# Optimization experiments

Measured on AMD Instinct MI355X. Metric: run time of the kernel, lower is better.

## Reference

```python
import jax, jax.numpy as jnp
import numpy as np

BNH, L, D = 32, 1024, 64        # (b*nh, seq_len, d_k)
CLIP = 64                        # rel_pos_clip
R = 2 * CLIP + 1                 # rel-pos table rows = 129
TEMP = 8.0                       # temperature = sqrt(d_k)


def setup_inputs() -> dict:
    key = jax.random.key(0)
    ks = jax.random.split(key, 7)
    q = jax.random.normal(ks[0], (BNH, L, D), jnp.float32)
    k = jax.random.normal(ks[1], (BNH, L, D), jnp.float32)
    v = jax.random.normal(ks[2], (BNH, L, D), jnp.float32)
    attn_w = jax.random.normal(ks[3], (BNH, L, L), jnp.float32)
    emb_k = jax.random.normal(ks[4], (R, D), jnp.float32)
    emb_v = jax.random.normal(ks[5], (R, D), jnp.float32)
    pos_seqs = jnp.sort(jax.random.randint(ks[6], (BNH, L), 0, 2048), axis=-1)
    mask = jnp.zeros((BNH, L, L), dtype=bool)  # no positions masked
    return {"q": q, "k": k, "v": v, "attn_w": attn_w,
            "emb_k": emb_k, "emb_v": emb_v,
            "pos_seqs": pos_seqs, "mask": mask}


def reference(q, k, v, attn_w, emb_k, emb_v, pos_seqs, mask):
    # relative-position index table: table[b,j,k] = clip(pos[k]-pos[j]) + CLIP, in [0, 2*CLIP]
    table = jnp.clip(pos_seqs[:, None, :] - pos_seqs[:, :, None], -CLIP, CLIP) + CLIP  # (bnh,l,l)

    # content scores
    attn = jnp.einsum('bid,bjd->bij', q, k)  # (bnh,l,l)

    # rel-pos key term: einsum('ijm,ijkm->ijk', q, emb_k[table]) done WITHOUT
    # materializing the (bnh,l,l,d) gather: project q onto all R embeddings,
    # then gather along the R axis (same math, far less memory traffic).
    qe = jnp.einsum('bid,rd->bir', q, emb_k)                 # (bnh,l,R)
    attn = attn + jnp.take_along_axis(qe, table, axis=2)     # (bnh,l,l)

    # score_util == 'np': additive posterior scores
    attn = attn + attn_w

    attn = attn / TEMP
    attn = jnp.where(mask, -jnp.inf, attn)
    p = jax.nn.softmax(attn, axis=2)
    # dropout is identity in eval mode

    out = jnp.einsum('bij,bjd->bid', p, v)                   # (bnh,l,d)

    # rel-pos value term: einsum('ijk,ijkm->ijm', p, emb_v[table]) via
    # scatter-add of probs into R buckets, then one small GEMM.
    bi = jnp.arange(BNH)[:, None, None]
    li = jnp.arange(L)[None, :, None]
    av = jnp.zeros((BNH, L, R), p.dtype).at[bi, li, table].add(p)  # (bnh,l,R)
    out = out + jnp.einsum('bir,rd->bid', av, emb_v)
    return out, p
```

## Files before the change

kernel.cpp:

```cpp
#include <hip/hip_runtime.h>

#define BNH 32
#define L 1024
#define D 64
#define RP 129
#define CLIPV 64
#define TI 16
#define TJ 128
#define NJT (L / TJ)
#define NT 256
#define SS 1032
#define KST 72
#define VST 136

typedef __attribute__((ext_vector_type(8))) short bf16x8;
typedef __attribute__((ext_vector_type(4))) float f32x4;
typedef __attribute__((ext_vector_type(8))) _Float16 f16x8;
typedef __attribute__((ext_vector_type(4))) _Float16 f16x4;

__device__ __forceinline__ unsigned short f2bf(float f) {
    unsigned int u = __builtin_bit_cast(unsigned int, f);
    return (unsigned short)((u + 0x7fffu + ((u >> 16) & 1u)) >> 16);
}

__global__ __launch_bounds__(NT, 2) void attn_fused(
    const float* __restrict__ q, const float* __restrict__ k, const float* __restrict__ v,
    const float* __restrict__ attn_w, const float* __restrict__ emb_k,
    const float* __restrict__ emb_v, const int* __restrict__ pos,
    const unsigned char* __restrict__ mask,
    float* __restrict__ out, float* __restrict__ p_out) {

    __shared__ __attribute__((aligned(16))) _Float16 s_lds[TI][SS];
    __shared__ __attribute__((aligned(16))) unsigned short kv_u[TJ * KST];
    __shared__ __attribute__((aligned(16))) unsigned short q_u[TI * KST];
    __shared__ unsigned short pos_s[L];
    __shared__ float qeav_s[TI * RP];
    __shared__ __attribute__((aligned(16))) float qfout_s[TI * 68];
    __shared__ float m_part[4][16];
    __shared__ float m_s[16];
    __shared__ float l_s[16];

    const int tid = threadIdx.x;
    const int wg = ((int)blockIdx.x & 7) * ((BNH * (L / TI)) >> 3) + ((int)blockIdx.x >> 3);
    const int b = wg >> 6;
    const int i0 = (wg & 63) * TI;
    const int w = tid >> 6;
    const int lane = tid & 63;
    const int quad = lane >> 4;
    const int lo = lane & 15;

    for (int t = tid; t < L; t += NT) pos_s[t] = (unsigned short)pos[b * L + t];
    {
        const int row = tid >> 4, c4 = tid & 15;
        *reinterpret_cast<float4*>(&qfout_s[row * 68 + c4 * 4]) =
            *reinterpret_cast<const float4*>(q + ((size_t)(b * L + i0 + row)) * D + c4 * 4);
    }
    if (tid < TI * 8) {
        const int r = tid >> 3, dc = tid & 7;
        const float* src = q + ((size_t)(b * L + i0 + r)) * D + dc * 8;
        float4 f0 = *(const float4*)src;
        float4 f1 = *(const float4*)(src + 4);
        bf16x8 qq;
        qq[0] = (short)f2bf(f0.x); qq[1] = (short)f2bf(f0.y);
        qq[2] = (short)f2bf(f0.z); qq[3] = (short)f2bf(f0.w);
        qq[4] = (short)f2bf(f1.x); qq[5] = (short)f2bf(f1.y);
        qq[6] = (short)f2bf(f1.z); qq[7] = (short)f2bf(f1.w);
        *(bf16x8*)&q_u[r * KST + dc * 8] = qq;
    }
    __syncthreads();

    {
        const int row = tid >> 4, rr = tid & 15;
        for (int r = rr; r < RP; r += 16) {
            float acc = 0.f;
#pragma unroll
            for (int d4 = 0; d4 < 16; ++d4) {
                float4 qv = *reinterpret_cast<const float4*>(&qfout_s[row * 68 + d4 * 4]);
                float4 ev = *reinterpret_cast<const float4*>(emb_k + r * D + d4 * 4);
                acc += qv.x * ev.x + qv.y * ev.y + qv.z * ev.z + qv.w * ev.w;
            }
            qeav_s[row * RP + r] = acc;
        }
    }
    __syncthreads();

    const bf16x8 aq0 = *(const bf16x8*)&q_u[lo * KST + quad * 8];
    const bf16x8 aq1 = *(const bf16x8*)&q_u[lo * KST + 32 + quad * 8];

    int posA[4];
#pragma unroll
    for (int r = 0; r < 4; ++r) posA[r] = (int)pos_s[i0 + quad * 4 + r];

    float mA[4] = {-3e38f, -3e38f, -3e38f, -3e38f};
    for (int jt = 0; jt < NJT; ++jt) {
        const int j0 = jt * TJ;
#pragma unroll
        for (int s = 0; s < 4; ++s) {
            int ch = s * NT + tid;
            int col = ch >> 3, dc = ch & 7;
            const float* src = k + ((size_t)(b * L + j0 + col)) * D + dc * 8;
            float4 f0 = *(const float4*)src;
            float4 f1 = *(const float4*)(src + 4);
            bf16x8 kk;
            kk[0] = (short)f2bf(f0.x); kk[1] = (short)f2bf(f0.y);
            kk[2] = (short)f2bf(f0.z); kk[3] = (short)f2bf(f0.w);
            kk[4] = (short)f2bf(f1.x); kk[5] = (short)f2bf(f1.y);
            kk[6] = (short)f2bf(f1.z); kk[7] = (short)f2bf(f1.w);
            *(bf16x8*)&kv_u[col * KST + dc * 8] = kk;
        }
        __syncthreads();
#pragma unroll
        for (int ct = 0; ct < 2; ++ct) {
            const int ncol = w * 32 + ct * 16 + lo;
            const int j = j0 + ncol;
            bf16x8 b0 = *(const bf16x8*)&kv_u[ncol * KST + quad * 8];
            bf16x8 b1 = *(const bf16x8*)&kv_u[ncol * KST + 32 + quad * 8];
            f32x4 acc = {0.f, 0.f, 0.f, 0.f};
            acc = __builtin_amdgcn_mfma_f32_16x16x32_bf16(aq0, b0, acc, 0, 0, 0);
            acc = __builtin_amdgcn_mfma_f32_16x16x32_bf16(aq1, b1, acc, 0, 0, 0);
            const int pj = (int)pos_s[j];
#pragma unroll
            for (int r = 0; r < 4; ++r) {
                const int row = quad * 4 + r;
                const size_t grow = (size_t)(b * L + i0 + row) * L + j;
                int dd = pj - posA[r];
                dd = min(max(dd, -CLIPV), CLIPV) + CLIPV;
                float sc = (acc[r] + qeav_s[row * RP + dd] + attn_w[grow]) * 0.125f;
                if (mask[grow]) sc = -3e38f;
                mA[r] = fmaxf(mA[r], sc);
                s_lds[row][j] = (_Float16)sc;
            }
        }
        __syncthreads();
    }

#pragma unroll
    for (int off = 1; off < 16; off <<= 1) {
#pragma unroll
        for (int r = 0; r < 4; ++r) mA[r] = fmaxf(mA[r], __shfl_xor(mA[r], off, 64));
    }
    if (lo == 0) {
#pragma unroll
        for (int r = 0; r < 4; ++r) m_part[w][quad * 4 + r] = mA[r];
    }
    __syncthreads();
    if (tid < 16) {
        m_s[tid] = fmaxf(fmaxf(m_part[0][tid], m_part[1][tid]),
                         fmaxf(m_part[2][tid], m_part[3][tid]));
        l_s[tid] = 0.f;
    }
    for (int t = tid; t < TI * RP; t += NT) qeav_s[t] = 0.f;
    for (int t = tid; t < TI * 68; t += NT) qfout_s[t] = 0.f;
    __syncthreads();

    const float mrow = m_s[lo];
    const int pos_m = (int)pos_s[i0 + lo];
    float l_r = 0.f;
    f32x4 oc[4];
#pragma unroll
    for (int ct = 0; ct < 4; ++ct) { oc[ct][0]=0.f; oc[ct][1]=0.f; oc[ct][2]=0.f; oc[ct][3]=0.f; }

    for (int jt = 0; jt < NJT; ++jt) {
        const int j0 = jt * TJ;
        const int colv = tid & 127, hv = tid >> 7;
        const float* srcv = v + ((size_t)(b * L + j0 + colv)) * D + hv * 32;
        float4 vf[8];
#pragma unroll
        for (int s = 0; s < 8; ++s) vf[s] = *(const float4*)(srcv + s * 4);
        __syncthreads();
#pragma unroll
        for (int s = 0; s < 8; ++s) {
            const int dbase = hv * 32 + s * 4;
            kv_u[(dbase + 0) * VST + colv] = f2bf(vf[s].x);
            kv_u[(dbase + 1) * VST + colv] = f2bf(vf[s].y);
            kv_u[(dbase + 2) * VST + colv] = f2bf(vf[s].z);
            kv_u[(dbase + 3) * VST + colv] = f2bf(vf[s].w);
        }
        __syncthreads();

        const int jcol = j0 + w * 32 + quad * 8;
        f16x8 sv = *reinterpret_cast<const f16x8*>(&s_lds[lo][jcol]);
        float ev[8];
#pragma unroll
        for (int i = 0; i < 8; ++i) ev[i] = __expf((float)sv[i] - mrow);
        l_r += ev[0] + ev[1] + ev[2] + ev[3] + ev[4] + ev[5] + ev[6] + ev[7];
        int cur = -1; float a = 0.f;
#pragma unroll
        for (int i = 0; i < 8; ++i) {
            int dd = (int)pos_s[jcol + i] - pos_m;
            dd = min(max(dd, -CLIPV), CLIPV) + CLIPV;
            if (dd != cur) {
                if (cur >= 0) atomicAdd(&qeav_s[lo * RP + cur], a);
                cur = dd; a = 0.f;
            }
            a += ev[i];
        }
        atomicAdd(&qeav_s[lo * RP + cur], a);
        bf16x8 af;
#pragma unroll
        for (int i = 0; i < 8; ++i) af[i] = (short)f2bf(ev[i]);
#pragma unroll
        for (int ct = 0; ct < 4; ++ct) {
            bf16x8 bf = *reinterpret_cast<const bf16x8*>(
                &kv_u[(ct * 16 + lo) * VST + w * 32 + quad * 8]);
            oc[ct] = __builtin_amdgcn_mfma_f32_16x16x32_bf16(af, bf, oc[ct], 0, 0, 0);
        }
    }

#pragma unroll
    for (int ct = 0; ct < 4; ++ct) {
#pragma unroll
        for (int r = 0; r < 4; ++r)
            atomicAdd(&qfout_s[(quad * 4 + r) * 68 + ct * 16 + lo], oc[ct][r]);
    }
    l_r += __shfl_xor(l_r, 16, 64);
    l_r += __shfl_xor(l_r, 32, 64);
    if (lane < 16) atomicAdd(&l_s[lo], l_r);
    __syncthreads();
    if (tid < 16) l_s[tid] = 1.f / l_s[tid];
    __syncthreads();

#pragma unroll
    for (int s = 0; s < TI; ++s) {
        f16x4 sv = *reinterpret_cast<const f16x4*>(&s_lds[s][tid * 4]);
        const float mm = m_s[s], il = l_s[s];
        float4 pv;
        pv.x = __expf((float)sv[0] - mm) * il;
        pv.y = __expf((float)sv[1] - mm) * il;
        pv.z = __expf((float)sv[2] - mm) * il;
        pv.w = __expf((float)sv[3] - mm) * il;
        *reinterpret_cast<float4*>(p_out + (size_t)(b * L + i0 + s) * L + tid * 4) = pv;
    }

    {
        const int row = tid >> 4, dc = tid & 15;
        float4 o = *(const float4*)&qfout_s[row * 68 + dc * 4];
        const float il = l_s[row];
        for (int r = 0; r < RP; ++r) {
            float a = qeav_s[row * RP + r];
            if (a != 0.f) {
                const float4 ev4 = *(const float4*)(emb_v + r * D + dc * 4);
                o.x += a * ev4.x; o.y += a * ev4.y;
                o.z += a * ev4.z; o.w += a * ev4.w;
            }
        }
        o.x *= il; o.y *= il; o.z *= il; o.w *= il;
        *(float4*)(out + (size_t)(b * L + i0 + row) * D + dc * 4) = o;
    }
}

extern "C" void kernel_launch(void* const* d_in, const int* in_sizes, int n_in,
                              void* d_out, int out_size, void* d_ws, size_t ws_size,
                              hipStream_t stream) {
    const float* q = (const float*)d_in[0];
    const float* k = (const float*)d_in[1];
    const float* v = (const float*)d_in[2];
    const float* attn_w = (const float*)d_in[3];
    const float* emb_k = (const float*)d_in[4];
    const float* emb_v = (const float*)d_in[5];
    const int* pos = (const int*)d_in[6];
    const unsigned char* mask = (const unsigned char*)d_in[7];
    float* out = (float*)d_out;
    float* p_out = out + (size_t)BNH * L * D;

    attn_fused<<<BNH * (L / TI), NT, 0, stream>>>(q, k, v, attn_w, emb_k, emb_v,
                                                  pos, mask, out, p_out);
}
```

Measured before the change: 647.6 us.

## Give each wave a private K/V tile with register double-buffering and cut shared memory

```diff
diff --git a/kernel.cpp b/kernel.cpp
--- a/kernel.cpp
+++ b/kernel.cpp
@@ -6,12 +6,12 @@
 #define RP 129
 #define CLIPV 64
 #define TI 16
-#define TJ 128
+#define TJ 64
 #define NJT (L / TJ)
 #define NT 256
 #define SS 1032
-#define KST 72
-#define VST 136
+#define KVST 72
+#define VTST 40
 
 typedef __attribute__((ext_vector_type(8))) short bf16x8;
 typedef __attribute__((ext_vector_type(4))) float f32x4;
@@ -23,22 +23,25 @@
     return (unsigned short)((u + 0x7fffu + ((u >> 16) & 1u)) >> 16);
 }
 
-__global__ __launch_bounds__(NT, 2) void attn_fused(
+__global__ __launch_bounds__(NT, 3) void attn_fused(
     const float* __restrict__ q, const float* __restrict__ k, const float* __restrict__ v,
     const float* __restrict__ attn_w, const float* __restrict__ emb_k,
     const float* __restrict__ emb_v, const int* __restrict__ pos,
     const unsigned char* __restrict__ mask,
     float* __restrict__ out, float* __restrict__ p_out) {
 
-    __shared__ __attribute__((aligned(16))) _Float16 s_lds[TI][SS];
-    __shared__ __attribute__((aligned(16))) unsigned short kv_u[TJ * KST];
-    __shared__ __attribute__((aligned(16))) unsigned short q_u[TI * KST];
-    __shared__ unsigned short pos_s[L];
-    __shared__ float qeav_s[TI * RP];
-    __shared__ __attribute__((aligned(16))) float qfout_s[TI * 68];
-    __shared__ float m_part[4][16];
-    __shared__ float m_s[16];
-    __shared__ float l_s[16];
+    __shared__ __attribute__((aligned(16))) char smem[53952];
+    _Float16* s_h = (_Float16*)smem;
+    float* qf = (float*)smem;
+    float* embv = (float*)smem;
+    unsigned short* kv = (unsigned short*)(smem + 33024);
+    float* buf0 = (float*)(smem + 33024);
+    float* buf1 = (float*)(smem + 37376);
+    float* qeav = (float*)(smem + 43264);
+    unsigned short* pos_s = (unsigned short*)(smem + 51520);
+    float* m_part = (float*)(smem + 53568);
+    float* m_s = (float*)(smem + 53824);
+    float* l_s = (float*)(smem + 53888);
 
     const int tid = threadIdx.x;
     const int wg = ((int)blockIdx.x & 7) * ((BNH * (L / TI)) >> 3) + ((int)blockIdx.x >> 3);
@@ -48,24 +51,13 @@
     const int lane = tid & 63;
     const int quad = lane >> 4;
     const int lo = lane & 15;
+    unsigned short* kvw = kv + w * 1280;
 
     for (int t = tid; t < L; t += NT) pos_s[t] = (unsigned short)pos[b * L + t];
     {
         const int row = tid >> 4, c4 = tid & 15;
-        *reinterpret_cast<float4*>(&qfout_s[row * 68 + c4 * 4]) =
+        *reinterpret_cast<float4*>(&qf[row * 68 + c4 * 4]) =
             *reinterpret_cast<const float4*>(q + ((size_t)(b * L + i0 + row)) * D + c4 * 4);
-    }
-    if (tid < TI * 8) {
-        const int r = tid >> 3, dc = tid & 7;
-        const float* src = q + ((size_t)(b * L + i0 + r)) * D + dc * 8;
-        float4 f0 = *(const float4*)src;
-        float4 f1 = *(const float4*)(src + 4);
-        bf16x8 qq;
-        qq[0] = (short)f2bf(f0.x); qq[1] = (short)f2bf(f0.y);
-        qq[2] = (short)f2bf(f0.z); qq[3] = (short)f2bf(f0.w);
-        qq[4] = (short)f2bf(f1.x); qq[5] = (short)f2bf(f1.y);
-        qq[6] = (short)f2bf(f1.z); qq[7] = (short)f2bf(f1.w);
-        *(bf16x8*)&q_u[r * KST + dc * 8] = qq;
     }
     __syncthreads();
 
@@ -75,63 +67,96 @@
             float acc = 0.f;
 #pragma unroll
             for (int d4 = 0; d4 < 16; ++d4) {
-                float4 qv = *reinterpret_cast<const float4*>(&qfout_s[row * 68 + d4 * 4]);
+                float4 qv = *reinterpret_cast<const float4*>(&qf[row * 68 + d4 * 4]);
                 float4 ev = *reinterpret_cast<const float4*>(emb_k + r * D + d4 * 4);
                 acc += qv.x * ev.x + qv.y * ev.y + qv.z * ev.z + qv.w * ev.w;
             }
-            qeav_s[row * RP + r] = acc;
-        }
-    }
-    __syncthreads();
-
-    const bf16x8 aq0 = *(const bf16x8*)&q_u[lo * KST + quad * 8];
-    const bf16x8 aq1 = *(const bf16x8*)&q_u[lo * KST + 32 + quad * 8];
-
+            qeav[row * RP + r] = acc;
+        }
+    }
+
+    bf16x8 aq0, aq1;
+    {
+        const float* qrow = q + (size_t)(b * L + i0 + lo) * D + quad * 8;
+        float4 a0 = *(const float4*)qrow, a1 = *(const float4*)(qrow + 4);
+        float4 a2 = *(const float4*)(qrow + 32), a3 = *(const float4*)(qrow + 36);
+        aq0[0] = (short)f2bf(a0.x); aq0[1] = (short)f2bf(a0.y);
+        aq0[2] = (short)f2bf(a0.z); aq0[3] = (short)f2bf(a0.w);
+        aq0[4] = (short)f2bf(a1.x); aq0[5] = (short)f2bf(a1.y);
+        aq0[6] = (short)f2bf(a1.z); aq0[7] = (short)f2bf(a1.w);
+        aq1[0] = (short)f2bf(a2.x); aq1[1] = (short)f2bf(a2.y);
+        aq1[2] = (short)f2bf(a2.z); aq1[3] = (short)f2bf(a2.w);
+        aq1[4] = (short)f2bf(a3.x); aq1[5] = (short)f2bf(a3.y);
+        aq1[6] = (short)f2bf(a3.z); aq1[7] = (short)f2bf(a3.w);
+    }
     int posA[4];
 #pragma unroll
     for (int r = 0; r < 4; ++r) posA[r] = (int)pos_s[i0 + quad * 4 + r];
+    __syncthreads();
 
     float mA[4] = {-3e38f, -3e38f, -3e38f, -3e38f};
-    for (int jt = 0; jt < NJT; ++jt) {
+
+    auto LOADA = [&](float4* kr, float* awr, int* mkr, int jt) {
         const int j0 = jt * TJ;
-#pragma unroll
-        for (int s = 0; s < 4; ++s) {
-            int ch = s * NT + tid;
-            int col = ch >> 3, dc = ch & 7;
-            const float* src = k + ((size_t)(b * L + j0 + col)) * D + dc * 8;
-            float4 f0 = *(const float4*)src;
-            float4 f1 = *(const float4*)(src + 4);
+        const int jj = j0 + w * 16 + lo;
+#pragma unroll
+        for (int r = 0; r < 4; ++r) {
+            const size_t grow = (size_t)(b * L + i0 + quad * 4 + r) * L + jj;
+            awr[r] = attn_w[grow];
+            mkr[r] = (int)mask[grow];
+        }
+#pragma unroll
+        for (int c = 0; c < 2; ++c) {
+            const int ch = c * 64 + lane;
+            const int col = ch >> 3, dc = ch & 7;
+            const float* src = k + ((size_t)(b * L + j0 + w * 16 + col)) * D + dc * 8;
+            kr[c * 2 + 0] = *(const float4*)src;
+            kr[c * 2 + 1] = *(const float4*)(src + 4);
+        }
+    };
+    auto PROCA = [&](const float4* kr, const float* awr, const int* mkr, int jt) {
+        const int j0 = jt * TJ;
+#pragma unroll
+        for (int c = 0; c < 2; ++c) {
+            const int ch = c * 64 + lane;
+            const int col = ch >> 3, dc = ch & 7;
             bf16x8 kk;
-            kk[0] = (short)f2bf(f0.x); kk[1] = (short)f2bf(f0.y);
-            kk[2] = (short)f2bf(f0.z); kk[3] = (short)f2bf(f0.w);
-            kk[4] = (short)f2bf(f1.x); kk[5] = (short)f2bf(f1.y);
-            kk[6] = (short)f2bf(f1.z); kk[7] = (short)f2bf(f1.w);
-            *(bf16x8*)&kv_u[col * KST + dc * 8] = kk;
-        }
-        __syncthreads();
-#pragma unroll
-        for (int ct = 0; ct < 2; ++ct) {
-            const int ncol = w * 32 + ct * 16 + lo;
-            const int j = j0 + ncol;
-            bf16x8 b0 = *(const bf16x8*)&kv_u[ncol * KST + quad * 8];
-            bf16x8 b1 = *(const bf16x8*)&kv_u[ncol * KST + 32 + quad * 8];
-            f32x4 acc = {0.f, 0.f, 0.f, 0.f};
-            acc = __builtin_amdgcn_mfma_f32_16x16x32_bf16(aq0, b0, acc, 0, 0, 0);
-            acc = __builtin_amdgcn_mfma_f32_16x16x32_bf16(aq1, b1, acc, 0, 0, 0);
-            const int pj = (int)pos_s[j];
-#pragma unroll
-            for (int r = 0; r < 4; ++r) {
-                const int row = quad * 4 + r;
-                const size_t grow = (size_t)(b * L + i0 + row) * L + j;
-                int dd = pj - posA[r];
-                dd = min(max(dd, -CLIPV), CLIPV) + CLIPV;
-                float sc = (acc[r] + qeav_s[row * RP + dd] + attn_w[grow]) * 0.125f;
-                if (mask[grow]) sc = -3e38f;
-                mA[r] = fmaxf(mA[r], sc);
-                s_lds[row][j] = (_Float16)sc;
-            }
-        }
-        __syncthreads();
+            kk[0] = (short)f2bf(kr[c * 2].x);     kk[1] = (short)f2bf(kr[c * 2].y);
+            kk[2] = (short)f2bf(kr[c * 2].z);     kk[3] = (short)f2bf(kr[c * 2].w);
+            kk[4] = (short)f2bf(kr[c * 2 + 1].x); kk[5] = (short)f2bf(kr[c * 2 + 1].y);
+            kk[6] = (short)f2bf(kr[c * 2 + 1].z); kk[7] = (short)f2bf(kr[c * 2 + 1].w);
+            *(bf16x8*)&kvw[col * KVST + dc * 8] = kk;
+        }
+        bf16x8 b0 = *(const bf16x8*)&kvw[lo * KVST + quad * 8];
+        bf16x8 b1 = *(const bf16x8*)&kvw[lo * KVST + 32 + quad * 8];
+        f32x4 acc = {0.f, 0.f, 0.f, 0.f};
+        acc = __builtin_amdgcn_mfma_f32_16x16x32_bf16(aq0, b0, acc, 0, 0, 0);
+        acc = __builtin_amdgcn_mfma_f32_16x16x32_bf16(aq1, b1, acc, 0, 0, 0);
+        const int j = j0 + w * 16 + lo;
+        const int pj = (int)pos_s[j];
+#pragma unroll
+        for (int r = 0; r < 4; ++r) {
+            const int row = quad * 4 + r;
+            int dd = pj - posA[r];
+            dd = min(max(dd, -CLIPV), CLIPV) + CLIPV;
+            float sc = (acc[r] + qeav[row * RP + dd] + awr[r]) * 0.125f;
+            if (mkr[r]) sc = -3e38f;
+            mA[r] = fmaxf(mA[r], sc);
+            s_h[row * SS + j] = (_Float16)sc;
+        }
+    };
+
+    {
+        float4 krA[4], krB[4];
+        float awA[4], awB[4];
+        int mkA[4], mkB[4];
+        LOADA(krA, awA, mkA, 0);
+        for (int jt = 0; jt < NJT; jt += 2) {
+            LOADA(krB, awB, mkB, jt + 1);
+            PROCA(krA, awA, mkA, jt);
+            if (jt + 2 < NJT) LOADA(krA, awA, mkA, jt + 2);
+            PROCA(krB, awB, mkB, jt + 1);
+        }
     }
 
 #pragma unroll
@@ -141,88 +166,95 @@
     }
     if (lo == 0) {
 #pragma unroll
-        for (int r = 0; r < 4; ++r) m_part[w][quad * 4 + r] = mA[r];
+        for (int r = 0; r < 4; ++r) m_part[w * 16 + quad * 4 + r] = mA[r];
     }
     __syncthreads();
     if (tid < 16) {
-        m_s[tid] = fmaxf(fmaxf(m_part[0][tid], m_part[1][tid]),
-                         fmaxf(m_part[2][tid], m_part[3][tid]));
+        m_s[tid] = fmaxf(fmaxf(m_part[tid], m_part[16 + tid]),
+                         fmaxf(m_part[32 + tid], m_part[48 + tid]));
         l_s[tid] = 0.f;
     }
-    for (int t = tid; t < TI * RP; t += NT) qeav_s[t] = 0.f;
-    for (int t = tid; t < TI * 68; t += NT) qfout_s[t] = 0.f;
+    for (int t = tid; t < TI * RP; t += NT) qeav[t] = 0.f;
     __syncthreads();
 
     const float mrow = m_s[lo];
     const int pos_m = (int)pos_s[i0 + lo];
     float l_r = 0.f;
-    f32x4 oc[4];
-#pragma unroll
-    for (int ct = 0; ct < 4; ++ct) { oc[ct][0]=0.f; oc[ct][1]=0.f; oc[ct][2]=0.f; oc[ct][3]=0.f; }
-
-    for (int jt = 0; jt < NJT; ++jt) {
-        const int j0 = jt * TJ;
-        const int colv = tid & 127, hv = tid >> 7;
-        const float* srcv = v + ((size_t)(b * L + j0 + colv)) * D + hv * 32;
-        float4 vf[8];
-#pragma unroll
-        for (int s = 0; s < 8; ++s) vf[s] = *(const float4*)(srcv + s * 4);
-        __syncthreads();
-#pragma unroll
-        for (int s = 0; s < 8; ++s) {
-            const int dbase = hv * 32 + s * 4;
-            kv_u[(dbase + 0) * VST + colv] = f2bf(vf[s].x);
-            kv_u[(dbase + 1) * VST + colv] = f2bf(vf[s].y);
-            kv_u[(dbase + 2) * VST + colv] = f2bf(vf[s].z);
-            kv_u[(dbase + 3) * VST + colv] = f2bf(vf[s].w);
-        }
-        __syncthreads();
-
-        const int jcol = j0 + w * 32 + quad * 8;
-        f16x8 sv = *reinterpret_cast<const f16x8*>(&s_lds[lo][jcol]);
+    f32x4 oc[2];
+    oc[0][0]=0.f; oc[0][1]=0.f; oc[0][2]=0.f; oc[0][3]=0.f;
+    oc[1][0]=0.f; oc[1][1]=0.f; oc[1][2]=0.f; oc[1][3]=0.f;
+    const int jhw = (w & 1) * 32, dhw = (w >> 1) * 32;
+
+    auto LOADB = [&](float4* vr, int jt) {
+        const int j0 = jt * TJ + jhw;
+#pragma unroll
+        for (int c = 0; c < 4; ++c) {
+            const int ch = c * 64 + lane;
+            const int jl = ch >> 3, c4 = ch & 7;
+            vr[c] = *(const float4*)(v + ((size_t)(b * L + j0 + jl)) * D + dhw + c4 * 4);
+        }
+    };
+    auto PROCB = [&](const float4* vr, int jt) {
+#pragma unroll
+        for (int c = 0; c < 4; ++c) {
+            const int ch = c * 64 + lane;
+            const int jl = ch >> 3, c4 = ch & 7;
+            kvw[(c4 * 4 + 0) * VTST + jl] = f2bf(vr[c].x);
+            kvw[(c4 * 4 + 1) * VTST + jl] = f2bf(vr[c].y);
+            kvw[(c4 * 4 + 2) * VTST + jl] = f2bf(vr[c].z);
+            kvw[(c4 * 4 + 3) * VTST + jl] = f2bf(vr[c].w);
+        }
+        const int jcol = jt * TJ + jhw + quad * 8;
+        f16x8 sv = *(const f16x8*)&s_h[lo * SS + jcol];
         float ev[8];
 #pragma unroll
         for (int i = 0; i < 8; ++i) ev[i] = __expf((float)sv[i] - mrow);
-        l_r += ev[0] + ev[1] + ev[2] + ev[3] + ev[4] + ev[5] + ev[6] + ev[7];
-        int cur = -1; float a = 0.f;
-#pragma unroll
-        for (int i = 0; i < 8; ++i) {
-            int dd = (int)pos_s[jcol + i] - pos_m;
-            dd = min(max(dd, -CLIPV), CLIPV) + CLIPV;
-            if (dd != cur) {
-                if (cur >= 0) atomicAdd(&qeav_s[lo * RP + cur], a);
-                cur = dd; a = 0.f;
+        if (w < 2) {
+            l_r += ev[0] + ev[1] + ev[2] + ev[3] + ev[4] + ev[5] + ev[6] + ev[7];
+            int cur = -1; float a = 0.f;
+#pragma unroll
+            for (int i = 0; i < 8; ++i) {
+                int dd = (int)pos_s[jcol + i] - pos_m;
+                dd = min(max(dd, -CLIPV), CLIPV) + CLIPV;
+                if (dd != cur) {
+                    if (cur >= 0) atomicAdd(&qeav[lo * RP + cur], a);
+                    cur = dd; a = 0.f;
+                }
+                a += ev[i];
             }
-            a += ev[i];
-        }
-        atomicAdd(&qeav_s[lo * RP + cur], a);
+            atomicAdd(&qeav[lo * RP + cur], a);
+        }
         bf16x8 af;
 #pragma unroll
         for (int i = 0; i < 8; ++i) af[i] = (short)f2bf(ev[i]);
 #pragma unroll
-        for (int ct = 0; ct < 4; ++ct) {
-            bf16x8 bf = *reinterpret_cast<const bf16x8*>(
-                &kv_u[(ct * 16 + lo) * VST + w * 32 + quad * 8]);
+        for (int ct = 0; ct < 2; ++ct) {
+            bf16x8 bf = *(const bf16x8*)&kvw[(ct * 16 + lo) * VTST + quad * 8];
             oc[ct] = __builtin_amdgcn_mfma_f32_16x16x32_bf16(af, bf, oc[ct], 0, 0, 0);
         }
-    }
-
-#pragma unroll
-    for (int ct = 0; ct < 4; ++ct) {
-#pragma unroll
-        for (int r = 0; r < 4; ++r)
-            atomicAdd(&qfout_s[(quad * 4 + r) * 68 + ct * 16 + lo], oc[ct][r]);
-    }
+    };
+
+    {
+        float4 vrA[4], vrB[4];
+        LOADB(vrA, 0);
+        for (int jt = 0; jt < NJT; jt += 2) {
+            LOADB(vrB, jt + 1);
+            PROCB(vrA, jt);
+            if (jt + 2 < NJT) LOADB(vrA, jt + 2);
+            PROCB(vrB, jt + 1);
+        }
+    }
+
     l_r += __shfl_xor(l_r, 16, 64);
     l_r += __shfl_xor(l_r, 32, 64);
-    if (lane < 16) atomicAdd(&l_s[lo], l_r);
+    if (w < 2 && lane < 16) atomicAdd(&l_s[lo], l_r);
     __syncthreads();
     if (tid < 16) l_s[tid] = 1.f / l_s[tid];
     __syncthreads();
 
 #pragma unroll
     for (int s = 0; s < TI; ++s) {
-        f16x4 sv = *reinterpret_cast<const f16x4*>(&s_lds[s][tid * 4]);
+        f16x4 sv = *reinterpret_cast<const f16x4*>(&s_h[s * SS + tid * 4]);
         const float mm = m_s[s], il = l_s[s];
         float4 pv;
         pv.x = __expf((float)sv[0] - mm) * il;
@@ -231,18 +263,37 @@
         pv.w = __expf((float)sv[3] - mm) * il;
         *reinterpret_cast<float4*>(p_out + (size_t)(b * L + i0 + s) * L + tid * 4) = pv;
     }
+    __syncthreads();
+
+    for (int t = tid; t < RP * 16; t += NT) {
+        const int r = t >> 4, c4 = t & 15;
+        *reinterpret_cast<float4*>(&embv[r * 64 + c4 * 4]) =
+            *reinterpret_cast<const float4*>(emb_v + r * D + c4 * 4);
+    }
+    {
+        float* bufw = (w & 1) ? buf1 : buf0;
+#pragma unroll
+        for (int ct = 0; ct < 2; ++ct) {
+#pragma unroll
+            for (int r = 0; r < 4; ++r)
+                bufw[(quad * 4 + r) * 68 + dhw + ct * 16 + lo] = oc[ct][r];
+        }
+    }
+    __syncthreads();
 
     {
         const int row = tid >> 4, dc = tid & 15;
-        float4 o = *(const float4*)&qfout_s[row * 68 + dc * 4];
+        float4 o0 = *(const float4*)&buf0[row * 68 + dc * 4];
+        float4 o1 = *(const float4*)&buf1[row * 68 + dc * 4];
+        float4 o;
+        o.x = o0.x + o1.x; o.y = o0.y + o1.y; o.z = o0.z + o1.z; o.w = o0.w + o1.w;
         const float il = l_s[row];
+#pragma unroll 4
         for (int r = 0; r < RP; ++r) {
-            float a = qeav_s[row * RP + r];
-            if (a != 0.f) {
-                const float4 ev4 = *(const float4*)(emb_v + r * D + dc * 4);
-                o.x += a * ev4.x; o.y += a * ev4.y;
-                o.z += a * ev4.z; o.w += a * ev4.w;
-            }
+            const float a = qeav[row * RP + r];
+            const float4 ev4 = *(const float4*)&embv[r * 64 + dc * 4];
+            o.x += a * ev4.x; o.y += a * ev4.y;
+            o.z += a * ev4.z; o.w += a * ev4.w;
         }
         o.x *= il; o.y *= il; o.z *= il; o.w *= il;
         *(float4*)(out + (size_t)(b * L + i0 + row) * D + dc * 4) = o;
```

After: 538.3 us. -16.9%, faster.
